# Optimization experiments

Measured on AMD Instinct MI355X. Metric: run time of the kernel, lower is better.

## Reference

```python
import jax, jax.numpy as jnp
import numpy as np
from jax import lax

B, T, SDIM, ADIM, HDIM, NH, NBLK, MAXT = 4, 512, 64, 32, 512, 8, 6, 4096
DFF = 4 * HDIM
S = 3 * T  # (num_state_tokens + 1) * context_len
DH = HDIM // NH


def _layernorm(x, g, b, eps=1e-5):
    m = jnp.mean(x, axis=-1, keepdims=True)
    v = jnp.mean((x - m) ** 2, axis=-1, keepdims=True)
    return (x - m) * lax.rsqrt(v + eps) * g + b


def setup_inputs() -> dict:
    key = jax.random.key(0)
    ks = iter(jax.random.split(key, 40))

    def nrm(shape, scale=0.02):
        return jax.random.normal(next(ks), shape, jnp.float32) * scale

    inp = {
        "timesteps": jax.random.randint(next(ks), (B, T), 0, MAXT),
        "state_0": jax.random.normal(next(ks), (B, T, SDIM), jnp.float32),
        "state_1": jax.random.normal(next(ks), (B, T, SDIM), jnp.float32),
        "actions": jax.random.normal(next(ks), (B, T, ADIM), jnp.float32),
        # embeddings / input projections
        "time_emb": nrm((MAXT, HDIM)),
        "Ws": nrm((SDIM, HDIM)), "bs": jnp.zeros((HDIM,), jnp.float32),
        "Wa": nrm((ADIM, HDIM)), "ba": jnp.zeros((HDIM,), jnp.float32),
        # stacked per-block transformer params (leading axis = n_blocks)
        "Wq": nrm((NBLK, HDIM, HDIM)), "bq": jnp.zeros((NBLK, HDIM), jnp.float32),
        "Wk": nrm((NBLK, HDIM, HDIM)), "bk": jnp.zeros((NBLK, HDIM), jnp.float32),
        "Wv": nrm((NBLK, HDIM, HDIM)), "bv": jnp.zeros((NBLK, HDIM), jnp.float32),
        "Wo": nrm((NBLK, HDIM, HDIM)), "bo": jnp.zeros((NBLK, HDIM), jnp.float32),
        "W1": nrm((NBLK, HDIM, DFF)), "b1": jnp.zeros((NBLK, DFF), jnp.float32),
        "W2": nrm((NBLK, DFF, HDIM)), "b2": jnp.zeros((NBLK, HDIM), jnp.float32),
        "ln1_g": jnp.ones((NBLK, HDIM), jnp.float32), "ln1_b": jnp.zeros((NBLK, HDIM), jnp.float32),
        "ln2_g": jnp.ones((NBLK, HDIM), jnp.float32), "ln2_b": jnp.zeros((NBLK, HDIM), jnp.float32),
        # embed layernorm + action head
        "eln_g": jnp.ones((HDIM,), jnp.float32), "eln_b": jnp.zeros((HDIM,), jnp.float32),
        "Wp": nrm((HDIM, ADIM)), "bp": jnp.zeros((ADIM,), jnp.float32),
    }
    return inp


def reference(timesteps, state_0, state_1, actions, time_emb, Ws, bs, Wa, ba,
              Wq, bq, Wk, bk, Wv, bv, Wo, bo, W1, b1, W2, b2,
              ln1_g, ln1_b, ln2_g, ln2_b, eln_g, eln_b, Wp, bp):
    te = time_emb[timesteps]                       # (B, T, H)
    s0 = state_0 @ Ws + bs + te                    # shared state embedding
    s1 = state_1 @ Ws + bs + te
    ae = actions @ Wa + ba + te
    # interleave: (B, T, 3, H) -> (B, 3T, H), token order [s0, s1, a] per timestep
    h = jnp.stack([s0, s1, ae], axis=2).reshape(B, S, HDIM)
    h = _layernorm(h, eln_g, eln_b)

    causal = jnp.tril(jnp.ones((S, S), dtype=bool))
    scale = 1.0 / float(DH) ** 0.5

    def block(x, p):
        wq, bq_, wk, bk_, wv, bv_, wo, bo_, w1, b1_, w2, b2_, g1, be1, g2, be2 = p
        q = (x @ wq + bq_).reshape(B, S, NH, DH)
        k = (x @ wk + bk_).reshape(B, S, NH, DH)
        v = (x @ wv + bv_).reshape(B, S, NH, DH)
        scores = jnp.einsum('bihd,bjhd->bhij', q, k) * scale
        scores = jnp.where(causal, scores, -jnp.inf)
        attn = jax.nn.softmax(scores, axis=-1)
        ctx = jnp.einsum('bhij,bjhd->bihd', attn, v).reshape(B, S, HDIM)
        x = x + (ctx @ wo + bo_)
        x = _layernorm(x, g1, be1)
        mlp = jax.nn.gelu(x @ w1 + b1_, approximate=False) @ w2 + b2_
        x = _layernorm(x + mlp, g2, be2)
        return x, None

    h, _ = lax.scan(block, h,
                    (Wq, bq, Wk, bk, Wv, bv, Wo, bo, W1, b1, W2, b2,
                     ln1_g, ln1_b, ln2_g, ln2_b))

    h = h.reshape(B, T, 3, HDIM)                   # (B, T, num_tokens, H)
    act_in = h[:, :, 1]                            # token index -2 = last state token
    return act_in @ Wp + bp                        # (B, T, act_dim)
```

## Files before the change

kernel.cpp:

```cpp
#include <hip/hip_runtime.h>
#include <hip/hip_bf16.h>
#include <math.h>

#define BB 4
#define TT 512
#define SDIM 64
#define ADIM 32
#define HDIM 512
#define NH 8
#define NBLK 6
#define DFF 2048
#define SS 1536
#define DH 64
#define MS (BB*SS)
#define SZE ((size_t)MS * HDIM)

typedef __attribute__((ext_vector_type(8))) __bf16 bf16x8;
typedef __attribute__((ext_vector_type(4))) float f32x4;

__device__ __forceinline__ __bf16 f2b(float x) { return (__bf16)x; }

__device__ __forceinline__ void gll16(const void* g, void* l) {
    __builtin_amdgcn_global_load_lds(
        (const __attribute__((address_space(1))) unsigned int*)g,
        (__attribute__((address_space(3))) unsigned int*)l, 16, 0, 0);
}

__global__ __launch_bounds__(512) void embed_ln_kernel(
    const int* __restrict__ timesteps,
    const float* __restrict__ state0, const float* __restrict__ state1,
    const float* __restrict__ actions, const float* __restrict__ time_emb,
    const float* __restrict__ Ws, const float* __restrict__ bs,
    const float* __restrict__ Wa, const float* __restrict__ ba,
    const float* __restrict__ eg, const float* __restrict__ eb,
    __bf16* __restrict__ h_bf)
{
    __shared__ float xs[8][64];
    __shared__ float acc_s[8][512];
    __shared__ int tss[8];
    int c = blockIdx.x, t = blockIdx.y, b = blockIdx.z;
    int i0 = c * 8;
    int tid = threadIdx.x;
    int K = (t == 2) ? ADIM : SDIM;
    int ksh = (t == 2) ? 5 : 6;
    const float* W    = (t == 2) ? Wa : Ws;
    const float* bias = (t == 2) ? ba : bs;
    const float* src  = (t == 0) ? state0  + ((size_t)(b*TT + i0)) * SDIM
                      : (t == 1) ? state1  + ((size_t)(b*TT + i0)) * SDIM
                                 : actions + ((size_t)(b*TT + i0)) * ADIM;

    if (tid < 8) tss[tid] = timesteps[b*TT + i0 + tid];
    for (int idx = tid; idx < 8 * K; idx += 512) {
        int r = idx >> ksh, kk = idx & (K - 1);
        xs[r][kk] = src[r * K + kk];
    }
    __syncthreads();

    float acc[8];
    #pragma unroll
    for (int r = 0; r < 8; ++r)
        acc[r] = bias[tid] + time_emb[(size_t)tss[r] * HDIM + tid];
    for (int kk = 0; kk < K; ++kk) {
        float w = W[(size_t)kk * HDIM + tid];
        #pragma unroll
        for (int r = 0; r < 8; ++r) acc[r] += xs[r][kk] * w;
    }
    #pragma unroll
    for (int r = 0; r < 8; ++r) acc_s[r][tid] = acc[r];
    __syncthreads();

    int w = tid >> 6, lane = tid & 63;
    float4 p0 = *(const float4*)&acc_s[w][lane * 8];
    float4 p1 = *(const float4*)&acc_s[w][lane * 8 + 4];
    float v[8] = {p0.x, p0.y, p0.z, p0.w, p1.x, p1.y, p1.z, p1.w};
    float s = 0.f, sq = 0.f;
    #pragma unroll
    for (int u = 0; u < 8; ++u) { s += v[u]; sq += v[u] * v[u]; }
    #pragma unroll
    for (int off = 1; off < 64; off <<= 1) { s += __shfl_xor(s, off); sq += __shfl_xor(sq, off); }
    float mean = s * (1.f / HDIM);
    float var  = sq * (1.f / HDIM) - mean * mean;
    float inv  = rsqrtf(var + 1e-5f);
    float4 g0 = *(const float4*)(eg + lane * 8), g1 = *(const float4*)(eg + lane * 8 + 4);
    float4 b0 = *(const float4*)(eb + lane * 8), b1 = *(const float4*)(eb + lane * 8 + 4);
    float gg[8] = {g0.x, g0.y, g0.z, g0.w, g1.x, g1.y, g1.z, g1.w};
    float bbv[8] = {b0.x, b0.y, b0.z, b0.w, b1.x, b1.y, b1.z, b1.w};
    __bf16 o8[8];
    #pragma unroll
    for (int u = 0; u < 8; ++u) o8[u] = f2b((v[u] - mean) * inv * gg[u] + bbv[u]);
    int row = b * SS + (i0 + w) * 3 + t;
    *(uint4*)(h_bf + (size_t)row * HDIM + lane * 8) = *(uint4*)o8;
}

template<int NP>
__global__ __launch_bounds__(256) void ln_add_kernel(
    __bf16* __restrict__ h_bf, const __bf16* __restrict__ parts,
    const float* __restrict__ g, const float* __restrict__ bvec)
{
    int w = threadIdx.x >> 6, lane = threadIdx.x & 63;
    int row = blockIdx.x * 4 + w;
    size_t base = (size_t)row * HDIM + lane * 8;
    bf16x8 h8 = *(const bf16x8*)(h_bf + base);
    bf16x8 p8[NP];
    #pragma unroll
    for (int p = 0; p < NP; ++p) p8[p] = *(const bf16x8*)(parts + p * SZE + base);
    float v[8], s = 0.f, sq = 0.f;
    #pragma unroll
    for (int u = 0; u < 8; ++u) {
        float acc = (float)h8[u];
        #pragma unroll
        for (int p = 0; p < NP; ++p) acc += (float)p8[p][u];
        v[u] = acc;
        s += acc; sq += acc * acc;
    }
    #pragma unroll
    for (int off = 1; off < 64; off <<= 1) { s += __shfl_xor(s, off); sq += __shfl_xor(sq, off); }
    float mean = s * (1.f / HDIM);
    float var  = sq * (1.f / HDIM) - mean * mean;
    float inv  = rsqrtf(var + 1e-5f);
    float4 g0 = *(const float4*)(g + lane * 8), g1 = *(const float4*)(g + lane * 8 + 4);
    float4 b0 = *(const float4*)(bvec + lane * 8), b1 = *(const float4*)(bvec + lane * 8 + 4);
    float gg[8] = {g0.x, g0.y, g0.z, g0.w, g1.x, g1.y, g1.z, g1.w};
    float bbv[8] = {b0.x, b0.y, b0.z, b0.w, b1.x, b1.y, b1.z, b1.w};
    __bf16 o8[8];
    #pragma unroll
    for (int u = 0; u < 8; ++u) o8[u] = f2b((v[u] - mean) * inv * gg[u] + bbv[u]);
    *(uint4*)(h_bf + base) = *(uint4*)o8;
}

__global__ __launch_bounds__(256) void pack_kernel(
    const float* __restrict__ Wq, const float* __restrict__ Wk,
    const float* __restrict__ Wv, const float* __restrict__ Wo,
    const float* __restrict__ W1, const float* __restrict__ W2,
    const float* __restrict__ bq_, const float* __restrict__ bk_, const float* __restrict__ bv_,
    __bf16* __restrict__ wqkvT, __bf16* __restrict__ woT,
    __bf16* __restrict__ w1T, __bf16* __restrict__ w2T, float* __restrict__ biasq)
{
    int lyr = blockIdx.y;
    const float* wq = Wq + (size_t)lyr * HDIM * HDIM;
    const float* wk = Wk + (size_t)lyr * HDIM * HDIM;
    const float* wv = Wv + (size_t)lyr * HDIM * HDIM;
    const float* wo = Wo + (size_t)lyr * HDIM * HDIM;
    const float* w1 = W1 + (size_t)lyr * HDIM * DFF;
    const float* w2 = W2 + (size_t)lyr * DFF * HDIM;
    const float* bqL = bq_ + (size_t)lyr * HDIM;
    const float* bkL = bk_ + (size_t)lyr * HDIM;
    const float* bvL = bv_ + (size_t)lyr * HDIM;
    wqkvT += (size_t)lyr * 1536 * 512;
    woT   += (size_t)lyr * 512 * 512;
    w1T   += (size_t)lyr * 2048 * 512;
    w2T   += (size_t)lyr * 512 * 2048;
    biasq += (size_t)lyr * 1536;

    int bid = blockIdx.x;
    int tid = threadIdx.x;
    if (bid == 768) {
        for (int i = tid; i < 1536; i += 256)
            biasq[i] = (i < 512) ? bqL[i] : ((i < 1024) ? bkL[i-512] : bvL[i-1024]);
        return;
    }
    __shared__ float Ls[64][65];
    const float* src; __bf16* dst; int K, N, kt, nt;
    if (bid < 192) {
        int sec = bid / 64, t = bid % 64;
        src = (sec == 0) ? wq : (sec == 1) ? wk : wv;
        dst = wqkvT + (size_t)sec * 512 * 512;
        K = 512; N = 512; nt = t >> 3; kt = t & 7;
    } else if (bid < 256) {
        int t = bid - 192; src = wo; dst = woT; K = 512; N = 512; nt = t >> 3; kt = t & 7;
    } else if (bid < 512) {
        int t = bid - 256; src = w1; dst = w1T; K = 512; N = 2048; nt = t >> 3; kt = t & 7;
    } else {
        int t = bid - 512; src = w2; dst = w2T; K = 2048; N = 512; nt = t & 7; kt = t >> 3;
    }
    int k0 = kt * 64, n0 = nt * 64;
    int rr = tid >> 4, cc = (tid & 15) * 4;
    #pragma unroll
    for (int p = 0; p < 4; ++p) {
        float4 v = *(const float4*)(src + (size_t)(k0 + rr + p*16) * N + n0 + cc);
        Ls[rr + p*16][cc] = v.x; Ls[rr + p*16][cc+1] = v.y;
        Ls[rr + p*16][cc+2] = v.z; Ls[rr + p*16][cc+3] = v.w;
    }
    __syncthreads();
    int nn = tid >> 3, kc = (tid & 7) * 8;
    #pragma unroll
    for (int p = 0; p < 2; ++p) {
        __bf16 t8[8];
        #pragma unroll
        for (int t2 = 0; t2 < 8; ++t2) t8[t2] = f2b(Ls[kc + t2][nn + p*32]);
        *(uint4*)(dst + (size_t)(n0 + nn + p*32) * K + k0 + kc) = *(uint4*)t8;
    }
}

template<int MT, bool VTMODE>
__global__ __launch_bounds__(256) void gemm_mfma(
    const __bf16* __restrict__ A, const __bf16* __restrict__ Bt,
    const float* __restrict__ bias, __bf16* __restrict__ C,
    __bf16* __restrict__ VTout,
    int N, int Ksub, int lda, int ldb, int ldc, int gelu, size_t cSplitStride)
{
    constexpr int MI = MT / 32;
    constexpr int SMB = 2*MT*64 + 2*128*64;
    __shared__ __align__(16) char sm[SMB];
    __bf16* As = (__bf16*)sm;
    __bf16* Bs = (__bf16*)(sm + 2*MT*64);
    int tid = threadIdx.x;
    int wave = tid >> 6, lane = tid & 63;
    int l15 = lane & 15, quad = lane >> 4;
    int wy = wave >> 1, wx = wave & 1;
    int m0 = blockIdx.y * MT, n0 = blockIdx.x * 128;
    int zs = blockIdx.z;
    int kbase = zs * Ksub;
    C += (size_t)zs * cSplitStride;

    int srow = lane >> 2;
    int clog = (lane & 3) ^ ((lane >> 3) & 3);
    int pchunk = (quad ^ ((l15 >> 1) & 3)) * 8;

    f32x4 acc[MI][4];
    #pragma unroll
    for (int i = 0; i < MI; ++i)
        #pragma unroll
        for (int j = 0; j < 4; ++j) acc[i][j] = (f32x4){0.f,0.f,0.f,0.f};

    const __bf16* Abase = A  + (size_t)m0 * lda + kbase + clog * 8;
    const __bf16* Bbase = Bt + (size_t)n0 * ldb + kbase + clog * 8;
    int NK = Ksub >> 5;

    #pragma unroll
    for (int q = 0; q < MT/64; ++q) {
        int r0 = (wave * (MT/64) + q) * 16;
        gll16(Abase + (size_t)(r0 + srow) * lda, As + r0*32);
    }
    #pragma unroll
    for (int q = 0; q < 2; ++q) {
        int r0 = (wave * 2 + q) * 16;
        gll16(Bbase + (size_t)(r0 + srow) * ldb, Bs + r0*32);
    }

    for (int kt = 0; kt < NK; ++kt) {
        int buf = kt & 1;
        __syncthreads();
        if (kt + 1 < NK) {
            int k0 = (kt + 1) << 5;
            #pragma unroll
            for (int q = 0; q < MT/64; ++q) {
                int r0 = (wave * (MT/64) + q) * 16;
                gll16(Abase + (size_t)(r0 + srow) * lda + k0, As + ((buf^1)*MT + r0)*32);
            }
            #pragma unroll
            for (int q = 0; q < 2; ++q) {
                int r0 = (wave * 2 + q) * 16;
                gll16(Bbase + (size_t)(r0 + srow) * ldb + k0, Bs + ((buf^1)*128 + r0)*32);
            }
        }
        bf16x8 af[MI], bf[4];
        #pragma unroll
        for (int i = 0; i < MI; ++i)
            af[i] = *(const bf16x8*)&As[(buf*MT + wy*(MT/2) + i*16 + l15)*32 + pchunk];
        #pragma unroll
        for (int j = 0; j < 4; ++j)
            bf[j] = *(const bf16x8*)&Bs[(buf*128 + wx*64 + j*16 + l15)*32 + pchunk];
        #pragma unroll
        for (int i = 0; i < MI; ++i)
            #pragma unroll
            for (int j = 0; j < 4; ++j)
                acc[i][j] = __builtin_amdgcn_mfma_f32_16x16x32_bf16(af[i], bf[j], acc[i][j], 0, 0, 0);
    }

    if (VTMODE && n0 >= 1024) {
        __syncthreads();
        __bf16* T = (__bf16*)sm;
        #pragma unroll
        for (int j = 0; j < 4; ++j) {
            int dl = wx*64 + j*16 + l15;
            float bv = bias[n0 + dl];
            int x31 = dl & 31;
            #pragma unroll
            for (int i = 0; i < MI; ++i) {
                int sc = wy*16 + i*4 + quad;
                int phys = sc ^ x31;
                __bf16 v4[4];
                #pragma unroll
                for (int r = 0; r < 4; ++r) v4[r] = f2b(acc[i][j][r] + bv);
                *(uint2*)(T + dl*128 + phys*4) = *(uint2*)v4;
            }
        }
        __syncthreads();
        int dl = tid >> 1, sh = (tid & 1) * 64;
        int dglob = n0 - 1024 + dl;
        int bb = m0 / SS, srel = m0 - bb*SS;
        __bf16* vb = VTout + ((size_t)(bb*NH + (dglob >> 6)) * 64 + (dglob & 63)) * SS + srel + sh;
        int x31 = dl & 31;
        #pragma unroll
        for (int u = 0; u < 8; ++u) {
            int c0 = (sh >> 2) + u*2;
            uint2 lo = *(const uint2*)(T + dl*128 + ((c0    ) ^ x31)*4);
            uint2 hi = *(const uint2*)(T + dl*128 + ((c0 + 1) ^ x31)*4);
            uint4 o; o.x = lo.x; o.y = lo.y; o.z = hi.x; o.w = hi.y;
            *(uint4*)(vb + u*8) = o;
        }
        return;
    }

    #pragma unroll
    for (int j = 0; j < 4; ++j) {
        int cc = n0 + wx*64 + j*16 + l15;
        float bv = (zs == 0) ? bias[cc] : 0.f;
        #pragma unroll
        for (int i = 0; i < MI; ++i) {
            #pragma unroll
            for (int r = 0; r < 4; ++r) {
                int rr = m0 + wy*(MT/2) + i*16 + quad*4 + r;
                float v = acc[i][j][r] + bv;
                if (gelu) {
                    float u2 = v * (0.7978845608f + 0.0356774081f * v * v);
                    float e  = __builtin_amdgcn_exp2f(u2 * 2.885390082f);
                    v = v * (1.f - __builtin_amdgcn_rcpf(e + 1.f));
                }
                C[(size_t)rr * ldc + cc] = f2b(v);
            }
        }
    }
}

#define SM_C 0.18033688011112042f

__device__ __forceinline__ unsigned pack2bf(float a, float b)
{
    union { __bf16 h[2]; unsigned u; } t;
    t.h[0] = (__bf16)a; t.h[1] = (__bf16)b;
    return t.u;
}

__device__ __forceinline__ bf16x8 ptrans(const float* p0, const float* p1, int lane)
{
    int l15 = lane & 15, quad = lane >> 4;
    unsigned pk0a = pack2bf(p0[0], p0[1]), pk0b = pack2bf(p0[2], p0[3]);
    unsigned pk1a = pack2bf(p1[0], p1[1]), pk1b = pack2bf(p1[2], p1[3]);
    int sA = l15 + (quad & 1) * 32;
    int sB = sA + 16;
    int hi = quad >> 1;
    unsigned a0A = (unsigned)__shfl((int)pk0a, sA);
    unsigned a1A = (unsigned)__shfl((int)pk1a, sA);
    unsigned b0A = (unsigned)__shfl((int)pk0b, sA);
    unsigned b1A = (unsigned)__shfl((int)pk1b, sA);
    unsigned a0B = (unsigned)__shfl((int)pk0a, sB);
    unsigned a1B = (unsigned)__shfl((int)pk1a, sB);
    unsigned b0B = (unsigned)__shfl((int)pk0b, sB);
    unsigned b1B = (unsigned)__shfl((int)pk1b, sB);
    union { unsigned u[4]; bf16x8 v; } pb;
    pb.u[0] = hi ? a1A : a0A;
    pb.u[1] = hi ? b1A : b0A;
    pb.u[2] = hi ? a1B : a0B;
    pb.u[3] = hi ? b1B : b0B;
    return pb.v;
}

__global__ __launch_bounds__(256, 3) void attn_kernel(
    __bf16* qkc, const __bf16* __restrict__ VT)
{
    __shared__ __align__(16) char smem[32768];

    int x = blockIdx.x;
    int region = x >> 8;
    int j = x & 255;
    int i = j >> 5;
    int hb = j & 31;
    int qt = (region == 0) ? (23 - i) : (region == 1) ? (8 + i) : i;
    int h = hb >> 2, b = hb & 3;

    int tid = threadIdx.x;
    int w = tid >> 6, lane = tid & 63;
    int l15 = lane & 15, quad = lane >> 4;
    int qrow0 = qt * 64 + w * 16;

    const __bf16* qp = qkc + (size_t)(b*SS + qrow0 + l15) * 1024 + h*64 + quad*8;
    bf16x8 qf0 = *(const bf16x8*)qp;
    bf16x8 qf1 = *(const bf16x8*)(qp + 32);

    const __bf16* kgbase = qkc + (size_t)(b*SS) * 1024 + 512 + h*64;
    const __bf16* vgbase = VT + (size_t)(b*NH + h) * 64 * SS;
    int srow8 = lane >> 3;
    int clog  = (lane & 7) ^ ((lane >> 3) & 7);
    int sw0 = ((0*4 + quad) ^ (l15 & 7)) * 8;
    int sw1 = ((1*4 + quad) ^ (l15 & 7)) * 8;

    f32x4 o0 = {0.f,0.f,0.f,0.f}, o1 = o0, o2 = o0, o3 = o0;
    float sm_m = -1e30f, sm_l = 0.f;

    int nkt = qt + 1;

    #pragma unroll
    for (int q = 0; q < 2; ++q) {
        int r0 = (w*2 + q) * 8;
        gll16(kgbase + (size_t)(r0 + srow8) * 1024 + clog*8, (__bf16*)smem + r0*64);
        gll16(vgbase + (size_t)(r0 + srow8) * SS   + clog*8, (__bf16*)(smem + 16384) + r0*64);
    }
    __syncthreads();

    for (int jt = 0; jt < nkt; ++jt) {
        int buf = jt & 1;
        const __bf16* Kb = (const __bf16*)(smem + buf * 8192);
        const __bf16* Vb = (const __bf16*)(smem + 16384 + buf * 8192);
        if (jt + 1 < nkt) {
            int kb2 = (jt + 1) * 64;
            __bf16* Kn = (__bf16*)(smem + (buf ^ 1) * 8192);
            __bf16* Vn = (__bf16*)(smem + 16384 + (buf ^ 1) * 8192);
            #pragma unroll
            for (int q = 0; q < 2; ++q) {
                int r0 = (w*2 + q) * 8;
                gll16(kgbase + (size_t)(kb2 + r0 + srow8) * 1024 + clog*8, Kn + r0*64);
                gll16(vgbase + (size_t)(r0 + srow8) * SS + kb2 + clog*8,   Vn + r0*64);
            }
        }
        int kb = jt * 64;

        f32x4 s[4];
        #pragma unroll
        for (int f = 0; f < 4; ++f) {
            bf16x8 k0 = *(const bf16x8*)(Kb + (16*f + l15)*64 + sw0);
            bf16x8 k1 = *(const bf16x8*)(Kb + (16*f + l15)*64 + sw1);
            f32x4 sf = {0.f,0.f,0.f,0.f};
            sf = __builtin_amdgcn_mfma_f32_16x16x32_bf16(k0, qf0, sf, 0, 0, 0);
            sf = __builtin_amdgcn_mfma_f32_16x16x32_bf16(k1, qf1, sf, 0, 0, 0);
            s[f] = sf;
        }

        if (kb + 63 > qrow0) {
            int qrow = qrow0 + l15;
            #pragma unroll
            for (int f = 0; f < 4; ++f)
                #pragma unroll
                for (int r = 0; r < 4; ++r)
                    if (kb + 16*f + quad*4 + r > qrow) s[f][r] = -1e30f;
        }

        float tf[4];
        #pragma unroll
        for (int f = 0; f < 4; ++f)
            tf[f] = fmaxf(fmaxf(s[f][0], s[f][1]), fmaxf(s[f][2], s[f][3]));
        float tm_lane = fmaxf(fmaxf(tf[0], tf[1]), fmaxf(tf[2], tf[3]));

        if (!__all(tm_lane <= sm_m + 64.f)) {
            float tm = tm_lane;
            tm = fmaxf(tm, __shfl_xor(tm, 16));
            tm = fmaxf(tm, __shfl_xor(tm, 32));
            float mnew = fmaxf(sm_m, tm);
            float alpha = __builtin_amdgcn_exp2f((sm_m - mnew) * SM_C);
            sm_l *= alpha;
            o0 *= alpha; o1 *= alpha; o2 *= alpha; o3 *= alpha;
            sm_m = mnew;
        }

        float negmC = -sm_m * SM_C;
        float pp[4][4];
        float rf[4];
        #pragma unroll
        for (int f = 0; f < 4; ++f) {
            #pragma unroll
            for (int r = 0; r < 4; ++r)
                pp[f][r] = __builtin_amdgcn_exp2f(fmaf(s[f][r], SM_C, negmC));
            rf[f] = (pp[f][0] + pp[f][1]) + (pp[f][2] + pp[f][3]);
        }
        sm_l += (rf[0] + rf[1]) + (rf[2] + rf[3]);

        bf16x8 pb01 = ptrans(pp[0], pp[1], lane);
        bf16x8 pb23 = ptrans(pp[2], pp[3], lane);

        #pragma unroll
        for (int ii = 0; ii < 4; ++ii) {
            bf16x8 va = *(const bf16x8*)(Vb + (16*ii + l15)*64 + sw0);
            bf16x8 vb = *(const bf16x8*)(Vb + (16*ii + l15)*64 + sw1);
            f32x4* op = (ii == 0) ? &o0 : (ii == 1) ? &o1 : (ii == 2) ? &o2 : &o3;
            *op = __builtin_amdgcn_mfma_f32_16x16x32_bf16(va, pb01, *op, 0, 0, 0);
            *op = __builtin_amdgcn_mfma_f32_16x16x32_bf16(vb, pb23, *op, 0, 0, 0);
        }
        __syncthreads();
    }

    sm_l += __shfl_xor(sm_l, 16);
    sm_l += __shfl_xor(sm_l, 32);
    float* otw = (float*)smem + w * 16 * 68;
    float inv = 1.f / sm_l;
    #pragma unroll
    for (int r = 0; r < 4; ++r) {
        otw[l15*68 +  0 + quad*4 + r] = o0[r] * inv;
        otw[l15*68 + 16 + quad*4 + r] = o1[r] * inv;
        otw[l15*68 + 32 + quad*4 + r] = o2[r] * inv;
        otw[l15*68 + 48 + quad*4 + r] = o3[r] * inv;
    }
    asm volatile("s_waitcnt lgkmcnt(0)" ::: "memory");
    int row = lane >> 2, ch = (lane & 3) * 16;
    union { __bf16 hh[16]; uint4 q4[2]; } ob;
    #pragma unroll
    for (int t2 = 0; t2 < 16; ++t2) ob.hh[t2] = f2b(otw[row*68 + ch + t2]);
    __bf16* cp = qkc + (size_t)(b*SS + qrow0 + row) * 1024 + h*64 + ch;
    *(uint4*)cp = ob.q4[0];
    *(uint4*)(cp + 8) = ob.q4[1];
}

__global__ __launch_bounds__(256) void proj_kernel(
    const __bf16* __restrict__ h_bf, const float* __restrict__ Wp,
    const float* __restrict__ bp, float* __restrict__ out)
{
    int rid = blockIdx.x * 8 + (threadIdx.x >> 5);
    int col = threadIdx.x & 31;
    int b = rid / TT, i = rid - b * TT;
    const __bf16* x = h_bf + ((size_t)(b*SS) + 3*i + 1) * HDIM;
    float acc = bp[col];
    for (int k8 = 0; k8 < HDIM/8; ++k8) {
        bf16x8 x8 = *(const bf16x8*)(x + k8*8);
        #pragma unroll
        for (int u = 0; u < 8; ++u)
            acc += (float)x8[u] * Wp[(k8*8 + u) * ADIM + col];
    }
    out[(size_t)rid * ADIM + col] = acc;
}

extern "C" void kernel_launch(void* const* d_in, const int* in_sizes, int n_in,
                              void* d_out, int out_size, void* d_ws, size_t ws_size,
                              hipStream_t stream)
{
    (void)in_sizes; (void)n_in; (void)out_size; (void)ws_size;
    const int*   timesteps = (const int*)  d_in[0];
    const float* state0    = (const float*)d_in[1];
    const float* state1    = (const float*)d_in[2];
    const float* actions   = (const float*)d_in[3];
    const float* time_emb  = (const float*)d_in[4];
    const float* Ws  = (const float*)d_in[5];
    const float* bs  = (const float*)d_in[6];
    const float* Wa  = (const float*)d_in[7];
    const float* ba  = (const float*)d_in[8];
    const float* Wq  = (const float*)d_in[9];
    const float* bq  = (const float*)d_in[10];
    const float* Wk  = (const float*)d_in[11];
    const float* bk  = (const float*)d_in[12];
    const float* Wv  = (const float*)d_in[13];
    const float* bv  = (const float*)d_in[14];
    const float* Wo  = (const float*)d_in[15];
    const float* bo  = (const float*)d_in[16];
    const float* W1  = (const float*)d_in[17];
    const float* b1  = (const float*)d_in[18];
    const float* W2  = (const float*)d_in[19];
    const float* b2  = (const float*)d_in[20];
    const float* ln1g = (const float*)d_in[21];
    const float* ln1b = (const float*)d_in[22];
    const float* ln2g = (const float*)d_in[23];
    const float* ln2b = (const float*)d_in[24];
    const float* elng = (const float*)d_in[25];
    const float* elnb = (const float*)d_in[26];
    const float* Wp   = (const float*)d_in[27];
    const float* bp   = (const float*)d_in[28];
    float* out = (float*)d_out;

    char* p = (char*)d_ws;
    __bf16* h_bf = (__bf16*)p;           p += SZE * 2;
    __bf16* qk   = (__bf16*)p;           p += (size_t)MS * 1024 * 2;
    __bf16* VT   = (__bf16*)p;           p += SZE * 2;
                      p += SZE * 2;
    __bf16* tmp  = (__bf16*)p;           p += SZE * 2 * 4;
    __bf16* wqkvT = (__bf16*)p;          p += (size_t)NBLK * 1536 * 512 * 2;
    __bf16* woT   = (__bf16*)p;          p += (size_t)NBLK * 512 * 512 * 2;
    __bf16* w1T   = (__bf16*)p;          p += (size_t)NBLK * 2048 * 512 * 2;
    __bf16* w2T   = (__bf16*)p;          p += (size_t)NBLK * 512 * 2048 * 2;
    float*  biasq = (float*)p;           p += (size_t)NBLK * 1536 * 4;
    __bf16* hid   = qk;

    embed_ln_kernel<<<dim3(TT/8, 3, BB), 512, 0, stream>>>(timesteps, state0, state1, actions,
                                                           time_emb, Ws, bs, Wa, ba, elng, elnb, h_bf);

    pack_kernel<<<dim3(769, NBLK), 256, 0, stream>>>(Wq, Wk, Wv, Wo, W1, W2, bq, bk, bv,
                                                     wqkvT, woT, w1T, w2T, biasq);

    dim3 gQKV(1536/128, MS/128, 1);
    dim3 gWO (512/128,  MS/64, 2);
    dim3 gW2 (512/128,  MS/128, 4);
    dim3 gF1 (2048/128, MS/128, 1);

    for (int lyr = 0; lyr < NBLK; ++lyr) {
        const __bf16* wqkvT_l = wqkvT + (size_t)lyr * 1536 * 512;
        const __bf16* woT_l   = woT   + (size_t)lyr * 512 * 512;
        const __bf16* w1T_l   = w1T   + (size_t)lyr * 2048 * 512;
        const __bf16* w2T_l   = w2T   + (size_t)lyr * 512 * 2048;
        const float*  biasq_l = biasq + (size_t)lyr * 1536;

        gemm_mfma<128, true><<<gQKV, 256, 0, stream>>>(h_bf, wqkvT_l, biasq_l, qk, VT,
                                                       1536, 512, 512, 512, 1024, 0, 0);
        attn_kernel<<<dim3(768), 256, 0, stream>>>(qk, VT);
        gemm_mfma<64, false><<<gWO, 256, 0, stream>>>(qk, woT_l, bo + lyr*HDIM, tmp, nullptr,
                                                      512, 256, 1024, 512, 512, 0, SZE);
        ln_add_kernel<2><<<MS/4, 256, 0, stream>>>(h_bf, tmp,
                                                   ln1g + lyr*HDIM, ln1b + lyr*HDIM);
        gemm_mfma<128, false><<<gF1, 256, 0, stream>>>(h_bf, w1T_l, b1 + lyr*DFF, hid, nullptr,
                                                       2048, 512, 512, 512, 2048, 1, 0);
        gemm_mfma<128, false><<<gW2, 256, 0, stream>>>(hid, w2T_l, b2 + lyr*HDIM, tmp, nullptr,
                                                       512, 512, 2048, 2048, 512, 0, SZE);
        ln_add_kernel<4><<<MS/4, 256, 0, stream>>>(h_bf, tmp,
                                                   ln2g + lyr*HDIM, ln2b + lyr*HDIM);
    }

    proj_kernel<<<(BB*TT)/8, 256, 0, stream>>>(h_bf, Wp, bp, out);
}
```

Before: 945.9 us.

## Stage GEMM epilogue through LDS for coalesced stores; use 2-way split-K for W2

The GEMM epilogue now writes bias/GELU results into an LDS tile, then each thread stores contiguous 16-byte chunks to global memory instead of scattered 2-byte stores. The W2 projection switches from a 128-row tile with 4-way split-K to a 64-row tile with 2-way split-K, so the following layernorm sums two partials instead of four. This cuts uncoalesced write traffic and partial-sum traffic, at the cost of an extra barrier, more LDS per block, and longer K loops per W2 block.

```diff
diff --git a/kernel.cpp b/kernel.cpp
--- a/kernel.cpp
+++ b/kernel.cpp
@@ -200,7 +200,8 @@
     int N, int Ksub, int lda, int ldb, int ldc, int gelu, size_t cSplitStride)
 {
     constexpr int MI = MT / 32;
-    constexpr int SMB = 2*MT*64 + 2*128*64;
+    constexpr int SMB0 = 2*MT*64 + 2*128*64;
+    constexpr int SMB = (MT*132*2 > SMB0) ? MT*132*2 : SMB0;
     __shared__ __align__(16) char sm[SMB];
     __bf16* As = (__bf16*)sm;
     __bf16* Bs = (__bf16*)(sm + 2*MT*64);
@@ -303,24 +304,38 @@
         return;
     }
 
+    __syncthreads();
+    __bf16* T = (__bf16*)sm;
     #pragma unroll
     for (int j = 0; j < 4; ++j) {
-        int cc = n0 + wx*64 + j*16 + l15;
-        float bv = (zs == 0) ? bias[cc] : 0.f;
+        int cl = wx*64 + j*16 + l15;
+        float bv = (zs == 0) ? bias[n0 + cl] : 0.f;
         #pragma unroll
         for (int i = 0; i < MI; ++i) {
             #pragma unroll
             for (int r = 0; r < 4; ++r) {
-                int rr = m0 + wy*(MT/2) + i*16 + quad*4 + r;
+                int rr = wy*(MT/2) + i*16 + quad*4 + r;
                 float v = acc[i][j][r] + bv;
                 if (gelu) {
                     float u2 = v * (0.7978845608f + 0.0356774081f * v * v);
                     float e  = __builtin_amdgcn_exp2f(u2 * 2.885390082f);
                     v = v * (1.f - __builtin_amdgcn_rcpf(e + 1.f));
                 }
-                C[(size_t)rr * ldc + cc] = f2b(v);
+                T[rr*132 + cl] = f2b(v);
             }
         }
+    }
+    __syncthreads();
+    constexpr int TPR = 256 / MT;
+    constexpr int CPT = 128 / TPR;
+    int row = tid / TPR, cp = (tid % TPR) * CPT;
+    __bf16* gout = C + (size_t)(m0 + row) * ldc + n0 + cp;
+    #pragma unroll
+    for (int u = 0; u < CPT/8; ++u) {
+        uint2 a = *(const uint2*)&T[row*132 + cp + u*8];
+        uint2 b = *(const uint2*)&T[row*132 + cp + u*8 + 4];
+        uint4 o; o.x = a.x; o.y = a.y; o.z = b.x; o.w = b.y;
+        *(uint4*)(gout + u*8) = o;
     }
 }
 
@@ -559,7 +574,7 @@
     __bf16* qk   = (__bf16*)p;           p += (size_t)MS * 1024 * 2;
     __bf16* VT   = (__bf16*)p;           p += SZE * 2;
                       p += SZE * 2;
-    __bf16* tmp  = (__bf16*)p;           p += SZE * 2 * 4;
+    __bf16* tmp  = (__bf16*)p;           p += SZE * 2 * 2;
     __bf16* wqkvT = (__bf16*)p;          p += (size_t)NBLK * 1536 * 512 * 2;
     __bf16* woT   = (__bf16*)p;          p += (size_t)NBLK * 512 * 512 * 2;
     __bf16* w1T   = (__bf16*)p;          p += (size_t)NBLK * 2048 * 512 * 2;
@@ -574,8 +589,7 @@
                                                      wqkvT, woT, w1T, w2T, biasq);
 
     dim3 gQKV(1536/128, MS/128, 1);
-    dim3 gWO (512/128,  MS/64, 2);
-    dim3 gW2 (512/128,  MS/128, 4);
+    dim3 gO  (512/128,  MS/64, 2);
     dim3 gF1 (2048/128, MS/128, 1);
 
     for (int lyr = 0; lyr < NBLK; ++lyr) {
@@ -588,15 +602,15 @@
         gemm_mfma<128, true><<<gQKV, 256, 0, stream>>>(h_bf, wqkvT_l, biasq_l, qk, VT,
                                                        1536, 512, 512, 512, 1024, 0, 0);
         attn_kernel<<<dim3(768), 256, 0, stream>>>(qk, VT);
-        gemm_mfma<64, false><<<gWO, 256, 0, stream>>>(qk, woT_l, bo + lyr*HDIM, tmp, nullptr,
-                                                      512, 256, 1024, 512, 512, 0, SZE);
+        gemm_mfma<64, false><<<gO, 256, 0, stream>>>(qk, woT_l, bo + lyr*HDIM, tmp, nullptr,
+                                                     512, 256, 1024, 512, 512, 0, SZE);
         ln_add_kernel<2><<<MS/4, 256, 0, stream>>>(h_bf, tmp,
                                                    ln1g + lyr*HDIM, ln1b + lyr*HDIM);
         gemm_mfma<128, false><<<gF1, 256, 0, stream>>>(h_bf, w1T_l, b1 + lyr*DFF, hid, nullptr,
                                                        2048, 512, 512, 512, 2048, 1, 0);
-        gemm_mfma<128, false><<<gW2, 256, 0, stream>>>(hid, w2T_l, b2 + lyr*HDIM, tmp, nullptr,
-                                                       512, 512, 2048, 2048, 512, 0, SZE);
-        ln_add_kernel<4><<<MS/4, 256, 0, stream>>>(h_bf, tmp,
+        gemm_mfma<64, false><<<gO, 256, 0, stream>>>(hid, w2T_l, b2 + lyr*HDIM, tmp, nullptr,
+                                                     512, 1024, 2048, 2048, 512, 0, SZE);
+        ln_add_kernel<2><<<MS/4, 256, 0, stream>>>(h_bf, tmp,
                                                    ln2g + lyr*HDIM, ln2b + lyr*HDIM);
     }
 
```

Result: no change. 946.4 us (+0.1%).
